# Kernel tuning notes

Hardware: AMD Instinct MI355X
Metric: run time of the kernel (lower is better)

## Reference

```python
import jax, jax.numpy as jnp
import numpy as np

B, M, C = 8, 8192, 256   # batch, seeds, seed feature dim
F = 128                  # vote feature dim
P, K = 256, 32           # proposals, samples per group
CA, NCLS = 256, 10       # aggregated feat dim, classes
RADIUS = 0.3


def _lin(x, w, b):
    # 1x1 conv == pointwise linear; w: (out, in)
    return jnp.einsum('...c,oc->...o', x, w) + b


def _bnrelu(x, s, t):
    # eval-mode BatchNorm folded to per-channel affine, then ReLU
    return jnp.maximum(x * s + t, 0.0)


def _fps(xyz, npoint):
    # farthest point sampling; deterministic start at index 0
    Bb, N, _ = xyz.shape
    bidx = jnp.arange(Bb)

    def step(carry, _):
        distance, farthest = carry
        centroid = xyz[bidx, farthest][:, None, :]          # (B,1,2)
        d = jnp.sum((xyz - centroid) ** 2, -1)              # (B,N)
        distance = jnp.minimum(distance, d)
        return (distance, jnp.argmax(distance, -1)), farthest

    init = (jnp.full((Bb, N), 1e10, xyz.dtype), jnp.zeros((Bb,), jnp.int32))
    _, idx = jax.lax.scan(step, init, None, length=npoint)
    return jnp.transpose(idx)                               # (B, npoint)


def _ball_query(xyz, new_xyz, radius, nsample):
    # squared-distance cdist (monotone in euclid dist, so same sort order)
    N = xyz.shape[1]
    d2 = (jnp.sum(new_xyz ** 2, -1)[:, :, None]
          + jnp.sum(xyz ** 2, -1)[:, None, :]
          - 2.0 * jnp.einsum('bsd,bnd->bsn', new_xyz, xyz))  # (B,S,N)
    gidx = jnp.broadcast_to(jnp.arange(N), d2.shape)
    # out-of-radius points replaced by group_first (= index 0, as in source)
    gidx = jnp.where(d2 > radius * radius, 0, gidx)
    order = jnp.argsort(d2, axis=-1)
    return jnp.take_along_axis(gidx, order, axis=-1)[:, :, :nsample]


def _gather(points, idx):
    # points: (B,N,C); idx: (B,...) -> (B,...,C)
    return jax.vmap(lambda p, i: p[i])(points, idx)


def _forward(seed_xyz, seed_feats,
             v_off_w1, v_off_b1, v_off_s1, v_off_t1, v_off_w2, v_off_b2,
             v_ft_w1, v_ft_b1, v_ft_s1, v_ft_t1, v_ft_w2, v_ft_b2,
             a_w1, a_b1, a_s1, a_t1, a_w2, a_b2, a_s2, a_t2,
             p_w1, p_b1, p_s1, p_t1, p_w2, p_b2, p_s2, p_t2,
             obj_w, obj_b, cls_w, cls_b):
    # --- VotingModule (vote_factor=1) ---
    h = _bnrelu(_lin(seed_feats, v_off_w1, v_off_b1), v_off_s1, v_off_t1)
    offsets = _lin(h, v_off_w2, v_off_b2)                   # (B,M,2)
    g = _bnrelu(_lin(seed_feats, v_ft_w1, v_ft_b1), v_ft_s1, v_ft_t1)
    vote_feats = _lin(g, v_ft_w2, v_ft_b2)                  # (B,M,F)
    votes_xyz = seed_xyz + offsets                          # (B,M,2)

    # --- VoteAggregation ---
    fps_idx = _fps(votes_xyz, P)                            # (B,P)
    new_xyz = _gather(votes_xyz, fps_idx)                   # (B,P,2)
    gidx = _ball_query(votes_xyz, new_xyz, RADIUS, K)       # (B,P,K)
    gv = _gather(votes_xyz, gidx)                           # (B,P,K,2)
    gf = _gather(vote_feats, gidx)                          # (B,P,K,F)
    comb = jnp.concatenate([gv - new_xyz[:, :, None, :], gf], -1)  # (B,P,K,F+2)
    x = _bnrelu(_lin(comb, a_w1, a_b1), a_s1, a_t1)
    x = _bnrelu(_lin(x, a_w2, a_b2), a_s2, a_t2)
    pooled = jnp.max(x, axis=2)                             # (B,P,CA)

    # --- ProposalHead ---
    y = _bnrelu(_lin(pooled, p_w1, p_b1), p_s1, p_t1)
    y = _bnrelu(_lin(y, p_w2, p_b2), p_s2, p_t2)
    obj = _lin(y, obj_w, obj_b)[..., 0]                     # (B,P)
    cls = _lin(y, cls_w, cls_b)                             # (B,P,NCLS)
    return (new_xyz, obj, cls)


def setup_inputs() -> dict:
    key = jax.random.key(0)
    keys = iter(jax.random.split(key, 40))

    def w(shape):
        return (jax.random.normal(next(keys), shape) * 0.05).astype(jnp.float32)

    inp = {
        'seed_xyz': jax.random.uniform(next(keys), (B, M, 2), jnp.float32),
        'seed_feats': jax.random.normal(next(keys), (B, M, C), jnp.float32),
        # voting: offset branch
        'v_off_w1': w((C, C)), 'v_off_b1': w((C,)),
        'v_off_s1': 1.0 + w((C,)), 'v_off_t1': w((C,)),
        'v_off_w2': w((2, C)), 'v_off_b2': w((2,)),
        # voting: feature branch
        'v_ft_w1': w((C, C)), 'v_ft_b1': w((C,)),
        'v_ft_s1': 1.0 + w((C,)), 'v_ft_t1': w((C,)),
        'v_ft_w2': w((F, C)), 'v_ft_b2': w((F,)),
        # aggregation MLP
        'a_w1': w((CA, F + 2)), 'a_b1': w((CA,)),
        'a_s1': 1.0 + w((CA,)), 'a_t1': w((CA,)),
        'a_w2': w((CA, CA)), 'a_b2': w((CA,)),
        'a_s2': 1.0 + w((CA,)), 'a_t2': w((CA,)),
        # proposal head
        'p_w1': w((CA, CA)), 'p_b1': w((CA,)),
        'p_s1': 1.0 + w((CA,)), 'p_t1': w((CA,)),
        'p_w2': w((CA // 2, CA)), 'p_b2': w((CA // 2,)),
        'p_s2': 1.0 + w((CA // 2,)), 'p_t2': w((CA // 2,)),
        'obj_w': w((1, CA // 2)), 'obj_b': w((1,)),
        'cls_w': w((NCLS, CA // 2)), 'cls_b': w((NCLS,)),
    }
    return inp


def reference(seed_xyz, seed_feats,
              v_off_w1, v_off_b1, v_off_s1, v_off_t1, v_off_w2, v_off_b2,
              v_ft_w1, v_ft_b1, v_ft_s1, v_ft_t1, v_ft_w2, v_ft_b2,
              a_w1, a_b1, a_s1, a_t1, a_w2, a_b2, a_s2, a_t2,
              p_w1, p_b1, p_s1, p_t1, p_w2, p_b2, p_s2, p_t2,
              obj_w, obj_b, cls_w, cls_b):
    return _forward(seed_xyz, seed_feats,
                    v_off_w1, v_off_b1, v_off_s1, v_off_t1, v_off_w2, v_off_b2,
                    v_ft_w1, v_ft_b1, v_ft_s1, v_ft_t1, v_ft_w2, v_ft_b2,
                    a_w1, a_b1, a_s1, a_t1, a_w2, a_b2, a_s2, a_t2,
                    p_w1, p_b1, p_s1, p_t1, p_w2, p_b2, p_s2, p_t2,
                    obj_w, obj_b, cls_w, cls_b)
```

## Files before the change

kernel.cpp:

```cpp
#include <hip/hip_runtime.h>

typedef __attribute__((ext_vector_type(8))) short bf16x8;
typedef __attribute__((ext_vector_type(4))) float f32x4;
typedef unsigned short u16;
typedef unsigned int u32;
typedef unsigned long long u64;

#define DEV static __device__ __forceinline__
DEV u16 f2bf(float f) { u32 i = __float_as_uint(f); i += 0x7fffu + ((i >> 16) & 1u); return (u16)(i >> 16); }
DEV float bf2f(u16 u) { return __uint_as_float(((u32)u) << 16); }

constexpr int Mn = 8192;
constexpr int Pn = 256;
constexpr int Kn = 32;
constexpr float R2 = 0.09f;

__global__ __launch_bounds__(256) void k_voting_off(
    const float* __restrict__ sxyz,
    const float* __restrict__ sfeat,
    const float* __restrict__ ow1, const float* __restrict__ ob1,
    const float* __restrict__ os1, const float* __restrict__ ot1,
    const float* __restrict__ ow2, const float* __restrict__ ob2,
    float* __restrict__ votes)
{
  __shared__ float Xst[256][17];
  __shared__ float Hst[256][17];
  __shared__ float Wc[16][260];

  const int tid = threadIdx.x;
  const int row0 = blockIdx.x * 16;

  for (int i = tid; i < 16 * 256; i += 256) {
    int r = i >> 8, c = i & 255;
    Xst[c][r] = sfeat[(row0 + r) * 256 + c];
  }
  __syncthreads();

  const int rg = tid >> 6;
  const int ro = rg * 4;
  const int cg = tid & 63;

  float acc[4][4];
#pragma unroll
  for (int r = 0; r < 4; ++r)
#pragma unroll
    for (int j = 0; j < 4; ++j) acc[r][j] = 0.f;
  const int co = cg * 4;

  for (int kc = 0; kc < 16; ++kc) {
    __syncthreads();
    for (int i = tid; i < 256 * 16; i += 256) {
      int o = i >> 4, k = i & 15;
      Wc[k][o] = ow1[o * 256 + kc * 16 + k];
    }
    __syncthreads();
#pragma unroll
    for (int k = 0; k < 16; ++k) {
      const int kk = kc * 16 + k;
      float x[4], w[4];
#pragma unroll
      for (int r = 0; r < 4; ++r) x[r] = Xst[kk][ro + r];
#pragma unroll
      for (int j = 0; j < 4; ++j) w[j] = Wc[k][co + j];
#pragma unroll
      for (int r = 0; r < 4; ++r)
#pragma unroll
        for (int j = 0; j < 4; ++j)
          acc[r][j] = fmaf(x[r], w[j], acc[r][j]);
    }
  }
  __syncthreads();
#pragma unroll
  for (int j = 0; j < 4; ++j) {
    int o = co + j;
    float bb = ob1[o], ss = os1[o], tt = ot1[o];
#pragma unroll
    for (int r = 0; r < 4; ++r)
      Hst[o][ro + r] = fmaxf((acc[r][j] + bb) * ss + tt, 0.f);
  }
  __syncthreads();

  if (tid < 32) {
    int r = tid >> 1, o = tid & 1;
    float a = 0.f;
    for (int k = 0; k < 256; ++k)
      a = fmaf(Hst[k][r], ow2[o * 256 + k], a);
    a += ob2[o];
    int row = row0 + r;
    votes[row * 2 + o] = sxyz[row * 2 + o] + a;
  }
}

__global__ __launch_bounds__(256) void k_fps(
    const float* __restrict__ votes, float* __restrict__ nxyz,
    float* __restrict__ out)
{
  const int b = blockIdx.x, tid = threadIdx.x;
  const float* vb = votes + b * Mn * 2;
  __shared__ u64 slotp[2][4];
  __shared__ float slotx[2][4], sloty[2][4];
  __shared__ float histx[256], histy[256];

  float px[32], py[32], dist[32];
#pragma unroll
  for (int s = 0; s < 32; ++s) {
    int i = tid * 32 + s;
    float2 p = *(const float2*)&vb[i * 2];
    px[s] = p.x; py[s] = p.y; dist[s] = 1e10f;
  }
  float cx = vb[0], cy = vb[1];
  if (tid == 0) { histx[0] = cx; histy[0] = cy; }

  for (int it = 1; it < Pn; ++it) {
    float bd = -1.f; int bi = 0;
#pragma unroll
    for (int s = 0; s < 32; ++s) {
      float dx = px[s] - cx, dy = py[s] - cy;
      float d = fminf(dist[s], dx * dx + dy * dy);
      dist[s] = d;
      if (d > bd) { bd = d; bi = tid * 32 + s; }
    }
    u64 pk = ((u64)__float_as_uint(bd) << 32) | (u32)(~bi);
    float wx = px[bi & 31], wy = py[bi & 31];
    (void)wx; (void)wy;
    float cxw = px[0], cyw = py[0];
#pragma unroll
    for (int s = 0; s < 32; ++s) {
      bool win = (tid * 32 + s) == bi;
      cxw = win ? px[s] : cxw;
      cyw = win ? py[s] : cyw;
    }
#pragma unroll
    for (int off = 32; off > 0; off >>= 1) {
      u64 opk = __shfl_xor(pk, off);
      float ox = __shfl_xor(cxw, off);
      float oy = __shfl_xor(cyw, off);
      if (opk > pk) { pk = opk; cxw = ox; cyw = oy; }
    }
    const int buf = it & 1, wv = tid >> 6;
    if ((tid & 63) == 0) {
      slotp[buf][wv] = pk; slotx[buf][wv] = cxw; sloty[buf][wv] = cyw;
    }
    __syncthreads();
    u64 wp = slotp[buf][0];
    float nx = slotx[buf][0], ny = sloty[buf][0];
#pragma unroll
    for (int w = 1; w < 4; ++w) {
      u64 op = slotp[buf][w];
      if (op > wp) { wp = op; nx = slotx[buf][w]; ny = sloty[buf][w]; }
    }
    cx = nx; cy = ny;
    if (tid == 0) { histx[it] = nx; histy[it] = ny; }
  }
  __syncthreads();
  {
    float2 o2; o2.x = histx[tid]; o2.y = histy[tid];
    *(float2*)&nxyz[(b * Pn + tid) * 2] = o2;
    *(float2*)&out[(b * Pn + tid) * 2] = o2;
  }
}

__global__ __launch_bounds__(256) void k_ballq(
    const float* __restrict__ votes, const float* __restrict__ nxyz,
    int* __restrict__ gidx)
{
  const int bp = blockIdx.x, tid = threadIdx.x;
  const int b = bp >> 8;
  const float* vb = votes + b * Mn * 2;
  const float sx = nxyz[bp * 2], sy = nxyz[bp * 2 + 1];
  const float a = sx * sx + sy * sy;
  float d2[32];
#pragma unroll
  for (int s = 0; s < 32; ++s) {
    int i = tid * 32 + s;
    float x = vb[i * 2], y = vb[i * 2 + 1];
    d2[s] = (a + (x * x + y * y)) - 2.f * (sx * x + sy * y);
  }
  __shared__ float sd[4];
  __shared__ int si[4];
  __shared__ int swi;
  unsigned mask = 0;
  for (int kk = 0; kk < Kn; ++kk) {
    float bd = 3.4e38f; int bi = 0x7fffffff;
#pragma unroll
    for (int s = 0; s < 32; ++s)
      if (!((mask >> s) & 1u) && d2[s] < bd) { bd = d2[s]; bi = tid * 32 + s; }
#pragma unroll
    for (int off = 32; off > 0; off >>= 1) {
      float od = __shfl_xor(bd, off);
      int oi = __shfl_xor(bi, off);
      if (od < bd || (od == bd && oi < bi)) { bd = od; bi = oi; }
    }
    if ((tid & 63) == 0) { sd[tid >> 6] = bd; si[tid >> 6] = bi; }
    __syncthreads();
    if (tid == 0) {
#pragma unroll
      for (int w = 1; w < 4; ++w)
        if (sd[w] < bd || (sd[w] == bd && si[w] < bi)) { bd = sd[w]; bi = si[w]; }
      swi = bi;
      gidx[bp * Kn + kk] = (bd > R2) ? 0 : bi;
    }
    __syncthreads();
    int wi = swi;
    if ((wi >> 5) == tid) mask |= 1u << (wi & 31);
  }
}

__global__ __launch_bounds__(256) void k_prep(
    const float* __restrict__ fw1, const float* __restrict__ fw2,
    const float* __restrict__ aw1, const float* __restrict__ aw2,
    u16* __restrict__ FW1h, u16* __restrict__ FW2b,
    u16* __restrict__ AW1b, u16* __restrict__ AW2b)
{
  const int gid = blockIdx.x * 256 + threadIdx.x;
  const int gsz = gridDim.x * 256;
  for (int i = gid; i < 65536; i += gsz) FW1h[i] = f2bf(fw1[i]);
  for (int i = gid; i < 32768; i += gsz) FW2b[i] = f2bf(fw2[i]);
  for (int i = gid; i < 65536; i += gsz) AW2b[i] = f2bf(aw2[i]);
  for (int i = gid; i < 49152; i += gsz) {
    int o = i / 192, k = i % 192;
    AW1b[i] = (k < 130) ? f2bf(aw1[o * 130 + k]) : (u16)0;
  }
}

__global__ __launch_bounds__(256) void k_vf(
    const float* __restrict__ sfeat, const u16* __restrict__ FW1h,
    const float* __restrict__ fb1, const float* __restrict__ fs1,
    const float* __restrict__ ft1, const u16* __restrict__ FW2b,
    const float* __restrict__ fb2, u16* __restrict__ vfeat)
{
  __shared__ u16 Hs[128 * 136];
  __shared__ u16 As[128 * 40];
  __shared__ u16 Bs[128 * 40];
  const int tid = threadIdx.x;
  const int row0 = blockIdx.x * 128;
  const int wid = tid >> 6, lane = tid & 63, m16 = lane & 15, quad = lane >> 4;
  const int wr = wid >> 1, wc = wid & 1;
  const int sr = tid >> 1, sk = (tid & 1) * 16;

  f32x4 acc2[4][4];
#pragma unroll
  for (int mt = 0; mt < 4; ++mt)
#pragma unroll
    for (int nt = 0; nt < 4; ++nt) acc2[mt][nt] = (f32x4){0.f, 0.f, 0.f, 0.f};

  for (int h = 0; h < 2; ++h) {
    f32x4 acc[4][4];
#pragma unroll
    for (int mt = 0; mt < 4; ++mt)
#pragma unroll
      for (int nt = 0; nt < 4; ++nt) acc[mt][nt] = (f32x4){0.f, 0.f, 0.f, 0.f};

    for (int s = 0; s < 8; ++s) {
      __syncthreads();
      {
        const float* src = &sfeat[(row0 + sr) * 256 + s * 32 + sk];
        u32 packed[8];
#pragma unroll
        for (int q = 0; q < 4; ++q) {
          float4 v = *(const float4*)&src[q * 4];
          packed[q * 2]     = (u32)f2bf(v.x) | ((u32)f2bf(v.y) << 16);
          packed[q * 2 + 1] = (u32)f2bf(v.z) | ((u32)f2bf(v.w) << 16);
        }
        *(uint4*)&As[sr * 40 + sk]     = *(uint4*)&packed[0];
        *(uint4*)&As[sr * 40 + sk + 8] = *(uint4*)&packed[4];
        const u16* bsrc = &FW1h[(h * 128 + sr) * 256 + s * 32 + sk];
        *(uint4*)&Bs[sr * 40 + sk]     = *(const uint4*)&bsrc[0];
        *(uint4*)&Bs[sr * 40 + sk + 8] = *(const uint4*)&bsrc[8];
      }
      __syncthreads();
#pragma unroll
      for (int mt = 0; mt < 4; ++mt) {
        bf16x8 af = *(const bf16x8*)&As[(wr * 64 + mt * 16 + m16) * 40 + quad * 8];
#pragma unroll
        for (int nt = 0; nt < 4; ++nt) {
          bf16x8 bfr = *(const bf16x8*)&Bs[(wc * 64 + nt * 16 + m16) * 40 + quad * 8];
          acc[mt][nt] = __builtin_amdgcn_mfma_f32_16x16x32_bf16(af, bfr, acc[mt][nt], 0, 0, 0);
        }
      }
    }
    __syncthreads();
#pragma unroll
    for (int nt = 0; nt < 4; ++nt) {
      int colL = wc * 64 + nt * 16 + m16;
      int col = h * 128 + colL;
      float bb = fb1[col], ss = fs1[col], tt = ft1[col];
#pragma unroll
      for (int mt = 0; mt < 4; ++mt) {
        int rL = wr * 64 + mt * 16 + quad * 4;
#pragma unroll
        for (int r = 0; r < 4; ++r)
          Hs[(rL + r) * 136 + colL] = f2bf(fmaxf((acc[mt][nt][r] + bb) * ss + tt, 0.f));
      }
    }
    for (int s2 = 0; s2 < 4; ++s2) {
      __syncthreads();
      {
        const u16* bsrc = &FW2b[sr * 256 + h * 128 + s2 * 32 + sk];
        *(uint4*)&Bs[sr * 40 + sk]     = *(const uint4*)&bsrc[0];
        *(uint4*)&Bs[sr * 40 + sk + 8] = *(const uint4*)&bsrc[8];
      }
      __syncthreads();
#pragma unroll
      for (int mt = 0; mt < 4; ++mt) {
        bf16x8 af = *(const bf16x8*)&Hs[(wr * 64 + mt * 16 + m16) * 136 + s2 * 32 + quad * 8];
#pragma unroll
        for (int nt = 0; nt < 4; ++nt) {
          bf16x8 bfr = *(const bf16x8*)&Bs[(wc * 64 + nt * 16 + m16) * 40 + quad * 8];
          acc2[mt][nt] = __builtin_amdgcn_mfma_f32_16x16x32_bf16(af, bfr, acc2[mt][nt], 0, 0, 0);
        }
      }
    }
  }
#pragma unroll
  for (int nt = 0; nt < 4; ++nt) {
    int col = wc * 64 + nt * 16 + m16;
    float bb = fb2[col];
#pragma unroll
    for (int mt = 0; mt < 4; ++mt) {
      int rbase = row0 + wr * 64 + mt * 16 + quad * 4;
#pragma unroll
      for (int r = 0; r < 4; ++r)
        vfeat[(rbase + r) * 128 + col] = f2bf(acc2[mt][nt][r] + bb);
    }
  }
}

__global__ __launch_bounds__(256) void k_agg(
    const float* __restrict__ votes, const u16* __restrict__ vfeat,
    const float* __restrict__ nxyz, const int* __restrict__ gidx,
    const u16* __restrict__ AW1b, const float* __restrict__ ab1,
    const float* __restrict__ as1, const float* __restrict__ at1,
    const u16* __restrict__ AW2b, const float* __restrict__ ab2,
    const float* __restrict__ as2, const float* __restrict__ at2,
    float* __restrict__ pooled)
{
  __shared__ u16 U[32 * 264];
  __shared__ u16 Bs[256 * 72];
  __shared__ int gix[32];
  __shared__ float gvx[32], gvy[32];
  u16* CombA = U;
  u16* As = U;
  float* x2T = (float*)Bs;

  const int bp = blockIdx.x, tid = threadIdx.x, b = bp >> 8;
  if (tid < 32) {
    int g = gidx[bp * 32 + tid];
    gix[tid] = g;
    gvx[tid] = votes[(b * Mn + g) * 2];
    gvy[tid] = votes[(b * Mn + g) * 2 + 1];
  }
  __syncthreads();
  const float sx = nxyz[bp * 2], sy = nxyz[bp * 2 + 1];

  if (tid < 192) {
    int row = tid / 6, c = tid % 6;
    const u16* vsrc = &vfeat[(b * Mn + gix[row]) * 128];
    u16* dst = &CombA[row * 200 + c * 32];
    if (c == 0) {
      dst[0] = f2bf(gvx[row] - sx);
      dst[1] = f2bf(gvy[row] - sy);
      for (int k = 2; k < 32; ++k) dst[k] = vsrc[k - 2];
    } else if (c <= 3) {
      for (int k = 0; k < 32; ++k) dst[k] = vsrc[c * 32 + k - 2];
    } else if (c == 4) {
      dst[0] = vsrc[126]; dst[1] = vsrc[127];
      for (int k = 2; k < 32; ++k) dst[k] = 0;
    } else {
      for (int k = 0; k < 32; ++k) dst[k] = 0;
    }
  }

  const int wid = tid >> 6, lane = tid & 63, m16 = lane & 15, quad = lane >> 4;
  const int mt = wid & 1, nh = wid >> 1;

  f32x4 acc[8];
#pragma unroll
  for (int nt = 0; nt < 8; ++nt) acc[nt] = (f32x4){0.f, 0.f, 0.f, 0.f};
  for (int s = 0; s < 3; ++s) {
    __syncthreads();
    for (int i = tid; i < 4096; i += 256) {
      int n = i >> 4, c4 = i & 15;
      *(uint2*)&Bs[n * 72 + c4 * 4] = *(const uint2*)&AW1b[n * 192 + s * 64 + c4 * 4];
    }
    __syncthreads();
#pragma unroll
    for (int ks = 0; ks < 2; ++ks) {
      bf16x8 af = *(const bf16x8*)&CombA[(mt * 16 + m16) * 200 + s * 64 + ks * 32 + quad * 8];
#pragma unroll
      for (int nt = 0; nt < 8; ++nt) {
        bf16x8 bf_ = *(const bf16x8*)&Bs[(nh * 128 + nt * 16 + m16) * 72 + ks * 32 + quad * 8];
        acc[nt] = __builtin_amdgcn_mfma_f32_16x16x32_bf16(af, bf_, acc[nt], 0, 0, 0);
      }
    }
  }
  __syncthreads();
#pragma unroll
  for (int nt = 0; nt < 8; ++nt) {
    int col = nh * 128 + nt * 16 + m16;
    float bb = ab1[col], ss = as1[col], tt = at1[col];
#pragma unroll
    for (int r = 0; r < 4; ++r) {
      int samp = mt * 16 + quad * 4 + r;
      As[samp * 264 + col] = f2bf(fmaxf((acc[nt][r] + bb) * ss + tt, 0.f));
    }
  }

  f32x4 acc2[8];
#pragma unroll
  for (int nt = 0; nt < 8; ++nt) acc2[nt] = (f32x4){0.f, 0.f, 0.f, 0.f};
  for (int s = 0; s < 4; ++s) {
    __syncthreads();
    for (int i = tid; i < 4096; i += 256) {
      int n = i >> 4, c4 = i & 15;
      *(uint2*)&Bs[n * 72 + c4 * 4] = *(const uint2*)&AW2b[n * 256 + s * 64 + c4 * 4];
    }
    __syncthreads();
#pragma unroll
    for (int ks = 0; ks < 2; ++ks) {
      bf16x8 af = *(const bf16x8*)&As[(mt * 16 + m16) * 264 + s * 64 + ks * 32 + quad * 8];
#pragma unroll
      for (int nt = 0; nt < 8; ++nt) {
        bf16x8 bf_ = *(const bf16x8*)&Bs[(nh * 128 + nt * 16 + m16) * 72 + ks * 32 + quad * 8];
        acc2[nt] = __builtin_amdgcn_mfma_f32_16x16x32_bf16(af, bf_, acc2[nt], 0, 0, 0);
      }
    }
  }
  __syncthreads();
#pragma unroll
  for (int nt = 0; nt < 8; ++nt) {
    int col = nh * 128 + nt * 16 + m16;
    float bb = ab2[col], ss = as2[col], tt = at2[col];
#pragma unroll
    for (int r = 0; r < 4; ++r) {
      int samp = mt * 16 + quad * 4 + r;
      x2T[col * 33 + samp] = fmaxf((acc2[nt][r] + bb) * ss + tt, 0.f);
    }
  }
  __syncthreads();
  {
    float m = x2T[tid * 33];
#pragma unroll
    for (int s2 = 1; s2 < 32; ++s2) m = fmaxf(m, x2T[tid * 33 + s2]);
    pooled[bp * 256 + tid] = m;
  }
}

__global__ __launch_bounds__(256) void k_head(
    const float* __restrict__ pooled,
    const float* __restrict__ pw1, const float* __restrict__ pb1,
    const float* __restrict__ ps1, const float* __restrict__ pt1,
    const float* __restrict__ pw2, const float* __restrict__ pb2,
    const float* __restrict__ ps2, const float* __restrict__ pt2,
    const float* __restrict__ objw, const float* __restrict__ objb,
    const float* __restrict__ clsw, const float* __restrict__ clsb,
    float* __restrict__ out)
{
  __shared__ float xr[256], y1[256], y2[128];
  const int bp = blockIdx.x, tid = threadIdx.x;
  xr[tid] = pooled[bp * 256 + tid];
  __syncthreads();
  {
    float a = 0.f;
    for (int c = 0; c < 256; ++c) a = fmaf(xr[c], pw1[tid * 256 + c], a);
    a = (a + pb1[tid]) * ps1[tid] + pt1[tid];
    y1[tid] = fmaxf(a, 0.f);
  }
  __syncthreads();
  if (tid < 128) {
    float a = 0.f;
    for (int c = 0; c < 256; ++c) a = fmaf(y1[c], pw2[tid * 256 + c], a);
    a = (a + pb2[tid]) * ps2[tid] + pt2[tid];
    y2[tid] = fmaxf(a, 0.f);
  }
  __syncthreads();
  if (tid < 10) {
    float a = 0.f;
    for (int c = 0; c < 128; ++c) a = fmaf(y2[c], clsw[tid * 128 + c], a);
    out[6144 + bp * 10 + tid] = a + clsb[tid];
  } else if (tid == 10) {
    float a = 0.f;
    for (int c = 0; c < 128; ++c) a = fmaf(y2[c], objw[c], a);
    out[4096 + bp] = a + objb[0];
  }
}

extern "C" void kernel_launch(void* const* d_in, const int* in_sizes, int n_in,
                              void* d_out, int out_size, void* d_ws, size_t ws_size,
                              hipStream_t stream)
{
  (void)in_sizes; (void)n_in; (void)out_size; (void)ws_size;
  const float* sxyz  = (const float*)d_in[0];
  const float* sfeat = (const float*)d_in[1];
  const float* ow1 = (const float*)d_in[2];
  const float* ob1 = (const float*)d_in[3];
  const float* os1 = (const float*)d_in[4];
  const float* ot1 = (const float*)d_in[5];
  const float* ow2 = (const float*)d_in[6];
  const float* ob2 = (const float*)d_in[7];
  const float* fw1 = (const float*)d_in[8];
  const float* fb1 = (const float*)d_in[9];
  const float* fs1 = (const float*)d_in[10];
  const float* ft1 = (const float*)d_in[11];
  const float* fw2 = (const float*)d_in[12];
  const float* fb2 = (const float*)d_in[13];
  const float* aw1 = (const float*)d_in[14];
  const float* ab1 = (const float*)d_in[15];
  const float* as1 = (const float*)d_in[16];
  const float* at1 = (const float*)d_in[17];
  const float* aw2 = (const float*)d_in[18];
  const float* ab2 = (const float*)d_in[19];
  const float* as2 = (const float*)d_in[20];
  const float* at2 = (const float*)d_in[21];
  const float* pw1 = (const float*)d_in[22];
  const float* pb1 = (const float*)d_in[23];
  const float* ps1 = (const float*)d_in[24];
  const float* pt1 = (const float*)d_in[25];
  const float* pw2 = (const float*)d_in[26];
  const float* pb2 = (const float*)d_in[27];
  const float* ps2 = (const float*)d_in[28];
  const float* pt2 = (const float*)d_in[29];
  const float* objw = (const float*)d_in[30];
  const float* objb = (const float*)d_in[31];
  const float* clsw = (const float*)d_in[32];
  const float* clsb = (const float*)d_in[33];

  char* ws = (char*)d_ws;
  float* votes  = (float*)(ws + 0);
  u16*   vfeat  = (u16*)  (ws + 524288);
  float* nxyz   = (float*)(ws + 17301504);
  int*   gidxp  = (int*)  (ws + 17317888);
  float* pooled = (float*)(ws + 17580032);
  u16*   FW1h   = (u16*)  (ws + 19677184);
  u16*   FW2b   = (u16*)  (ws + 19808256);
  u16*   AW1b   = (u16*)  (ws + 19873792);
  u16*   AW2b   = (u16*)  (ws + 19972096);
  float* out    = (float*)d_out;

  k_voting_off<<<dim3(4096), dim3(256), 0, stream>>>(
      sxyz, sfeat, ow1, ob1, os1, ot1, ow2, ob2, votes);

  k_fps<<<dim3(8), dim3(256), 0, stream>>>(votes, nxyz, out);

  k_ballq<<<dim3(2048), dim3(256), 0, stream>>>(votes, nxyz, gidxp);

  k_prep<<<dim3(256), dim3(256), 0, stream>>>(
      fw1, fw2, aw1, aw2, FW1h, FW2b, AW1b, AW2b);

  k_vf<<<dim3(512), dim3(256), 0, stream>>>(
      sfeat, FW1h, fb1, fs1, ft1, FW2b, fb2, vfeat);

  k_agg<<<dim3(2048), dim3(256), 0, stream>>>(
      votes, vfeat, nxyz, gidxp, AW1b, ab1, as1, at1,
      AW2b, ab2, as2, at2, pooled);

  k_head<<<dim3(2048), dim3(256), 0, stream>>>(
      pooled, pw1, pb1, ps1, pt1, pw2, pb2, ps2, pt2,
      objw, objb, clsw, clsb, out);
}
```

Baseline: 1.030 ms.

## Speed up FPS reduction with DPP row reductions and 512-thread blocks

The farthest-point-sampling kernel now runs 512 threads per batch, each owning 16 points instead of 32. The per-iteration argmax reduction changes from 64-wide u64 shuffles plus a 4-way shared-memory step to 16-lane DPP row-rotate reductions. The winner's coordinates are carried along during the scan rather than found by a separate selection pass. The aim is to shorten the serial per-iteration critical path of the 255-step loop. In exchange, every thread redundantly reduces over 32 shared slots, and there are more waves per block to synchronise.

```diff
diff --git a/kernel.cpp b/kernel.cpp
--- a/kernel.cpp
+++ b/kernel.cpp
@@ -91,20 +91,19 @@
   }
 }
 
-__global__ __launch_bounds__(256) void k_fps(
+__global__ __launch_bounds__(512, 1) void k_fps(
     const float* __restrict__ votes, float* __restrict__ nxyz,
     float* __restrict__ out)
 {
   const int b = blockIdx.x, tid = threadIdx.x;
   const float* vb = votes + b * Mn * 2;
-  __shared__ u64 slotp[2][4];
-  __shared__ float slotx[2][4], sloty[2][4];
+  __shared__ uint4 slots[2][32];
   __shared__ float histx[256], histy[256];
 
-  float px[32], py[32], dist[32];
-#pragma unroll
-  for (int s = 0; s < 32; ++s) {
-    int i = tid * 32 + s;
+  float px[16], py[16], dist[16];
+#pragma unroll
+  for (int s = 0; s < 16; ++s) {
+    int i = tid * 16 + s;
     float2 p = *(const float2*)&vb[i * 2];
     px[s] = p.x; py[s] = p.y; dist[s] = 1e10f;
   }
@@ -112,48 +111,57 @@
   if (tid == 0) { histx[0] = cx; histy[0] = cy; }
 
   for (int it = 1; it < Pn; ++it) {
-    float bd = -1.f; int bi = 0;
-#pragma unroll
-    for (int s = 0; s < 32; ++s) {
+    float bd = -1.f; float bx = 0.f, by = 0.f; int bi = 0;
+#pragma unroll
+    for (int s = 0; s < 16; ++s) {
       float dx = px[s] - cx, dy = py[s] - cy;
       float d = fminf(dist[s], dx * dx + dy * dy);
       dist[s] = d;
-      if (d > bd) { bd = d; bi = tid * 32 + s; }
-    }
-    u64 pk = ((u64)__float_as_uint(bd) << 32) | (u32)(~bi);
-    float wx = px[bi & 31], wy = py[bi & 31];
-    (void)wx; (void)wy;
-    float cxw = px[0], cyw = py[0];
-#pragma unroll
-    for (int s = 0; s < 32; ++s) {
-      bool win = (tid * 32 + s) == bi;
-      cxw = win ? px[s] : cxw;
-      cyw = win ? py[s] : cyw;
-    }
-#pragma unroll
-    for (int off = 32; off > 0; off >>= 1) {
-      u64 opk = __shfl_xor(pk, off);
-      float ox = __shfl_xor(cxw, off);
-      float oy = __shfl_xor(cyw, off);
-      if (opk > pk) { pk = opk; cxw = ox; cyw = oy; }
-    }
-    const int buf = it & 1, wv = tid >> 6;
-    if ((tid & 63) == 0) {
-      slotp[buf][wv] = pk; slotx[buf][wv] = cxw; sloty[buf][wv] = cyw;
-    }
-    __syncthreads();
-    u64 wp = slotp[buf][0];
-    float nx = slotx[buf][0], ny = sloty[buf][0];
-#pragma unroll
-    for (int w = 1; w < 4; ++w) {
-      u64 op = slotp[buf][w];
-      if (op > wp) { wp = op; nx = slotx[buf][w]; ny = sloty[buf][w]; }
-    }
-    cx = nx; cy = ny;
-    if (tid == 0) { histx[it] = nx; histy[it] = ny; }
-  }
-  __syncthreads();
-  {
+      if (d > bd) { bd = d; bi = tid * 16 + s; bx = px[s]; by = py[s]; }
+    }
+    u32 hd = __float_as_uint(bd), hl = ~(u32)bi;
+    u32 hx = __float_as_uint(bx), hy = __float_as_uint(by);
+
+#define FPS_ROR(N)                                                              \
+    {                                                                           \
+      u32 od = (u32)__builtin_amdgcn_update_dpp(0, (int)hd, 0x120 + N, 0xF, 0xF, false); \
+      u32 ol = (u32)__builtin_amdgcn_update_dpp(0, (int)hl, 0x120 + N, 0xF, 0xF, false); \
+      u32 ox = (u32)__builtin_amdgcn_update_dpp(0, (int)hx, 0x120 + N, 0xF, 0xF, false); \
+      u32 oy = (u32)__builtin_amdgcn_update_dpp(0, (int)hy, 0x120 + N, 0xF, 0xF, false); \
+      bool g = (od > hd) || (od == hd && ol > hl);                              \
+      hd = g ? od : hd; hl = g ? ol : hl; hx = g ? ox : hx; hy = g ? oy : hy;   \
+    }
+    FPS_ROR(8) FPS_ROR(4) FPS_ROR(2) FPS_ROR(1)
+
+    const int buf = it & 1;
+    if ((tid & 15) == 0) slots[buf][tid >> 4] = make_uint4(hd, hl, hx, hy);
+    __syncthreads();
+
+    uint4 t0 = slots[buf][tid & 15];
+    uint4 t1 = slots[buf][16 + (tid & 15)];
+    {
+      bool g = (t1.x > t0.x) || (t1.x == t0.x && t1.y > t0.y);
+      if (g) t0 = t1;
+    }
+    u32 rd = t0.x, rl = t0.y, rx = t0.z, ry = t0.w;
+#define FPS_ROR2(N)                                                             \
+    {                                                                           \
+      u32 od = (u32)__builtin_amdgcn_update_dpp(0, (int)rd, 0x120 + N, 0xF, 0xF, false); \
+      u32 ol = (u32)__builtin_amdgcn_update_dpp(0, (int)rl, 0x120 + N, 0xF, 0xF, false); \
+      u32 ox = (u32)__builtin_amdgcn_update_dpp(0, (int)rx, 0x120 + N, 0xF, 0xF, false); \
+      u32 oy = (u32)__builtin_amdgcn_update_dpp(0, (int)ry, 0x120 + N, 0xF, 0xF, false); \
+      bool g = (od > rd) || (od == rd && ol > rl);                              \
+      rd = g ? od : rd; rl = g ? ol : rl; rx = g ? ox : rx; ry = g ? oy : ry;   \
+    }
+    FPS_ROR2(8) FPS_ROR2(4) FPS_ROR2(2) FPS_ROR2(1)
+#undef FPS_ROR
+#undef FPS_ROR2
+
+    cx = __uint_as_float(rx); cy = __uint_as_float(ry);
+    if (tid == 0) { histx[it] = cx; histy[it] = cy; }
+  }
+  __syncthreads();
+  if (tid < 256) {
     float2 o2; o2.x = histx[tid]; o2.y = histy[tid];
     *(float2*)&nxyz[(b * Pn + tid) * 2] = o2;
     *(float2*)&out[(b * Pn + tid) * 2] = o2;
@@ -540,7 +548,7 @@
   k_voting_off<<<dim3(4096), dim3(256), 0, stream>>>(
       sxyz, sfeat, ow1, ob1, os1, ot1, ow2, ob2, votes);
 
-  k_fps<<<dim3(8), dim3(256), 0, stream>>>(votes, nxyz, out);
+  k_fps<<<dim3(8), dim3(512), 0, stream>>>(votes, nxyz, out);
 
   k_ballq<<<dim3(2048), dim3(256), 0, stream>>>(votes, nxyz, gidxp);
 
```

After: 1.032 ms. About the same (+0.2%).

## Rework FPS argmax reduction with DPP row rotations and shared-memory second stage

Applied to the files above, without the earlier changes.

Restructures the farthest-point-sampling per-iteration argmax. Each thread now tracks its candidate coordinates inline across two independent halves, which removes the separate select loop over 32 registers. The cross-lane stage uses DPP row-rotate reductions within 16-lane rows, and a second DPP pass over the 16 row results written to shared memory replaces the 64-lane shuffle and serial 4-wave combine. It also pins point registers and sets launch bounds to one block per SM. The tie-breaking comparison on index must match the original lowest-index rule, and the reduction depends on DPP row semantics being correct.

```diff
diff --git a/kernel.cpp b/kernel.cpp
--- a/kernel.cpp
+++ b/kernel.cpp
@@ -91,14 +91,13 @@
   }
 }
 
-__global__ __launch_bounds__(256) void k_fps(
+__global__ __launch_bounds__(256, 1) void k_fps(
     const float* __restrict__ votes, float* __restrict__ nxyz,
     float* __restrict__ out)
 {
   const int b = blockIdx.x, tid = threadIdx.x;
   const float* vb = votes + b * Mn * 2;
-  __shared__ u64 slotp[2][4];
-  __shared__ float slotx[2][4], sloty[2][4];
+  __shared__ u32 S[2][4][16];
   __shared__ float histx[256], histy[256];
 
   float px[32], py[32], dist[32];
@@ -108,49 +107,68 @@
     float2 p = *(const float2*)&vb[i * 2];
     px[s] = p.x; py[s] = p.y; dist[s] = 1e10f;
   }
+#pragma unroll
+  for (int s = 0; s < 32; ++s) {
+    asm volatile("" : "+v"(px[s]), "+v"(py[s]));
+  }
   float cx = vb[0], cy = vb[1];
   if (tid == 0) { histx[0] = cx; histy[0] = cy; }
 
   for (int it = 1; it < Pn; ++it) {
-    float bd = -1.f; int bi = 0;
-#pragma unroll
-    for (int s = 0; s < 32; ++s) {
+    float bd0 = -1.f, bx0 = 0.f, by0 = 0.f; int bi0 = 0;
+    float bd1 = -1.f, bx1 = 0.f, by1 = 0.f; int bi1 = 0;
+#pragma unroll
+    for (int s = 0; s < 16; ++s) {
       float dx = px[s] - cx, dy = py[s] - cy;
       float d = fminf(dist[s], dx * dx + dy * dy);
       dist[s] = d;
-      if (d > bd) { bd = d; bi = tid * 32 + s; }
-    }
-    u64 pk = ((u64)__float_as_uint(bd) << 32) | (u32)(~bi);
-    float wx = px[bi & 31], wy = py[bi & 31];
-    (void)wx; (void)wy;
-    float cxw = px[0], cyw = py[0];
-#pragma unroll
-    for (int s = 0; s < 32; ++s) {
-      bool win = (tid * 32 + s) == bi;
-      cxw = win ? px[s] : cxw;
-      cyw = win ? py[s] : cyw;
-    }
-#pragma unroll
-    for (int off = 32; off > 0; off >>= 1) {
-      u64 opk = __shfl_xor(pk, off);
-      float ox = __shfl_xor(cxw, off);
-      float oy = __shfl_xor(cyw, off);
-      if (opk > pk) { pk = opk; cxw = ox; cyw = oy; }
-    }
-    const int buf = it & 1, wv = tid >> 6;
-    if ((tid & 63) == 0) {
-      slotp[buf][wv] = pk; slotx[buf][wv] = cxw; sloty[buf][wv] = cyw;
-    }
-    __syncthreads();
-    u64 wp = slotp[buf][0];
-    float nx = slotx[buf][0], ny = sloty[buf][0];
-#pragma unroll
-    for (int w = 1; w < 4; ++w) {
-      u64 op = slotp[buf][w];
-      if (op > wp) { wp = op; nx = slotx[buf][w]; ny = sloty[buf][w]; }
-    }
-    cx = nx; cy = ny;
-    if (tid == 0) { histx[it] = nx; histy[it] = ny; }
+      if (d > bd0) { bd0 = d; bi0 = tid * 32 + s; bx0 = px[s]; by0 = py[s]; }
+    }
+#pragma unroll
+    for (int s = 16; s < 32; ++s) {
+      float dx = px[s] - cx, dy = py[s] - cy;
+      float d = fminf(dist[s], dx * dx + dy * dy);
+      dist[s] = d;
+      if (d > bd1) { bd1 = d; bi1 = tid * 32 + s; bx1 = px[s]; by1 = py[s]; }
+    }
+    if (bd1 > bd0) { bd0 = bd1; bi0 = bi1; bx0 = bx1; by0 = by1; }
+
+    u32 hd = __float_as_uint(bd0), hl = ~(u32)bi0;
+    u32 hx = __float_as_uint(bx0), hy = __float_as_uint(by0);
+
+#define FPS_ROR(VD, VL, VX, VY, N)                                              \
+    {                                                                           \
+      u32 od = (u32)__builtin_amdgcn_update_dpp(0, (int)VD, 0x120 + N, 0xF, 0xF, false); \
+      u32 ol = (u32)__builtin_amdgcn_update_dpp(0, (int)VL, 0x120 + N, 0xF, 0xF, false); \
+      u32 ox = (u32)__builtin_amdgcn_update_dpp(0, (int)VX, 0x120 + N, 0xF, 0xF, false); \
+      u32 oy = (u32)__builtin_amdgcn_update_dpp(0, (int)VY, 0x120 + N, 0xF, 0xF, false); \
+      bool g = (od > VD) || (od == VD && ol > VL);                              \
+      VD = g ? od : VD; VL = g ? ol : VL; VX = g ? ox : VX; VY = g ? oy : VY;   \
+    }
+    FPS_ROR(hd, hl, hx, hy, 8)
+    FPS_ROR(hd, hl, hx, hy, 4)
+    FPS_ROR(hd, hl, hx, hy, 2)
+    FPS_ROR(hd, hl, hx, hy, 1)
+
+    const int buf = it & 1;
+    if ((tid & 15) == 0) {
+      int row = tid >> 4;
+      S[buf][0][row] = hd; S[buf][1][row] = hl;
+      S[buf][2][row] = hx; S[buf][3][row] = hy;
+    }
+    __syncthreads();
+
+    int rr = tid & 15;
+    u32 rd = S[buf][0][rr], rl = S[buf][1][rr];
+    u32 rx = S[buf][2][rr], ry = S[buf][3][rr];
+    FPS_ROR(rd, rl, rx, ry, 8)
+    FPS_ROR(rd, rl, rx, ry, 4)
+    FPS_ROR(rd, rl, rx, ry, 2)
+    FPS_ROR(rd, rl, rx, ry, 1)
+#undef FPS_ROR
+
+    cx = __uint_as_float(rx); cy = __uint_as_float(ry);
+    if (tid == 0) { histx[it] = cx; histy[it] = cy; }
   }
   __syncthreads();
   {
```

Measured after the change: 1.065 ms. 3.4% more time.
